# Kernel tuning notes

Hardware: AMD Instinct MI355X
Metric: run time of the kernel (lower is better)

Reference implementation:

```python
import jax, jax.numpy as jnp
import numpy as np

USER_NUM = 100000
ITEM_NUM = 50000
N_NODES = USER_NUM + ITEM_NUM
HIDE_DIM = 64
N_EDGES = 4000000
LAYER_NUM = 3


def setup_inputs() -> dict:
    key = jax.random.key(0)
    k1, k2, k3, k4 = jax.random.split(key, 4)
    # Xavier uniform for embeddings: bound = sqrt(6/(fan_in+fan_out))
    bound_u = float(np.sqrt(6.0 / (USER_NUM + HIDE_DIM)))
    bound_i = float(np.sqrt(6.0 / (ITEM_NUM + HIDE_DIM)))
    user_emb = jax.random.uniform(k1, (USER_NUM, HIDE_DIM), jnp.float32, -bound_u, bound_u)
    item_emb = jax.random.uniform(k2, (ITEM_NUM, HIDE_DIM), jnp.float32, -bound_i, bound_i)
    src = jax.random.randint(k3, (N_EDGES,), 0, N_NODES, dtype=jnp.int32)
    dst = jax.random.randint(k4, (N_EDGES,), 0, N_NODES, dtype=jnp.int32)
    return {"user_emb": user_emb, "item_emb": item_emb, "src": src, "dst": dst}


def _gcn_layer(node_f, src, dst, out_norm, in_norm):
    # node_f: [N, D]; symmetric degree-normalized SpMM (copy_u + sum)
    h = node_f * out_norm  # pre-scale by out_degree^-0.5
    agg = jax.ops.segment_sum(h[src], dst, num_segments=N_NODES)
    return agg * in_norm  # post-scale by in_degree^-0.5


def reference(user_emb, item_emb, src, dst):
    ones = jnp.ones((N_EDGES,), jnp.float32)
    out_deg = jnp.clip(jax.ops.segment_sum(ones, src, num_segments=N_NODES), 1.0)
    in_deg = jnp.clip(jax.ops.segment_sum(ones, dst, num_segments=N_NODES), 1.0)
    out_norm = (out_deg ** -0.5)[:, None]
    in_norm = (in_deg ** -0.5)[:, None]

    res_user = user_emb
    res_item = item_emb
    for i in range(LAYER_NUM):
        if i == 0:
            node_f = jnp.concatenate([res_user, res_item], axis=0)
        else:
            node_f = embeddings
        embeddings = _gcn_layer(node_f, src, dst, out_norm, in_norm)
        scale = 1.0 / (i + 2)
        res_user = res_user + embeddings[:USER_NUM] * scale
        res_item = res_item + embeddings[USER_NUM:] * scale
    return (res_user, res_item)
```

## Files before the change

kernel.cpp:

```cpp
#include <hip/hip_runtime.h>
#include <stdint.h>

#define USER_NUM 100000
#define ITEM_NUM 50000
#define N_NODES  150000
#define HIDE_DIM 64
#define N_EDGES  4000000
#define SLAB     72

#define HRANGES 3
#define RNODES  50000
#define RWORDS  (RNODES / 4)
#define SLICES  128
#define EPS     (N_EDGES / SLICES)

#define BSH     9
#define BNODES  512
#define NBUCK   293
#define SSLICES 640
#define EPSB    (N_EDGES / SSLICES)

__device__ __forceinline__ unsigned short f2bf(float f) {
    union { float f; unsigned int i; } c; c.f = f;
    unsigned int b = c.i;
    return (unsigned short)((b + 0x7FFFu + ((b >> 16) & 1u)) >> 16);
}
__device__ __forceinline__ float lo_bf(uint32_t u) {
    union { uint32_t u; float f; } c; c.u = u << 16; return c.f;
}
__device__ __forceinline__ float hi_bf(uint32_t u) {
    union { uint32_t u; float f; } c; c.u = u & 0xffff0000u; return c.f;
}

__global__ void histfused_kernel(const int* __restrict__ src, const int* __restrict__ dst,
                                 uint32_t* __restrict__ partial, uint32_t* __restrict__ btot) {
    __shared__ uint32_t bins[RWORDS];
    int r  = blockIdx.x / SLICES;
    int sl = blockIdx.x - r * SLICES;
    int e0 = sl * EPS, e1 = e0 + EPS;
    if (r < HRANGES) {
        for (int i = threadIdx.x; i < RWORDS; i += 512) bins[i] = 0;
        __syncthreads();
        int lo = r * RNODES, hi = lo + RNODES;
        for (int e = e0 + threadIdx.x; e < e1; e += 512) {
            int s = src[e];
            if (s >= lo && s < hi) {
                int x = s - lo;
                atomicAdd(&bins[x >> 2], 1u << (8 * (x & 3)));
            }
        }
        __syncthreads();
        uint32_t* out = partial + (size_t)(r * SLICES + sl) * RWORDS;
        for (int i = threadIdx.x; i < RWORDS; i += 512) out[i] = bins[i];
    } else {
        for (int i = threadIdx.x; i < NBUCK; i += 512) bins[i] = 0;
        __syncthreads();
        for (int e = e0 + threadIdx.x; e < e1; e += 512)
            atomicAdd(&bins[((unsigned)dst[e]) >> BSH], 1u);
        __syncthreads();
        for (int i = threadIdx.x; i < NBUCK; i += 512)
            if (bins[i]) atomicAdd(&btot[i], bins[i]);
    }
}

__global__ void rednorm_kernel(const uint32_t* __restrict__ partial, float* __restrict__ out_norm) {
    int g = blockIdx.x * blockDim.x + threadIdx.x;
    if (g >= HRANGES * RWORDS) return;
    int r = g / RWORDS, w = g - r * RWORDS;
    const uint32_t* p = partial + (size_t)r * SLICES * RWORDS + w;
    uint32_t acc = 0;
#pragma unroll 16
    for (int sl = 0; sl < SLICES; ++sl) acc += p[(size_t)sl * RWORDS];
    int oc0 = acc & 255, oc1 = (acc >> 8) & 255, oc2 = (acc >> 16) & 255, oc3 = (acc >> 24);
    float4 o;
    o.x = 1.0f / sqrtf((float)(oc0 < 1 ? 1 : oc0));
    o.y = 1.0f / sqrtf((float)(oc1 < 1 ? 1 : oc1));
    o.z = 1.0f / sqrtf((float)(oc2 < 1 ? 1 : oc2));
    o.w = 1.0f / sqrtf((float)(oc3 < 1 ? 1 : oc3));
    ((float4*)out_norm)[(size_t)r * (RNODES / 4) + w] = o;
}

__global__ void scatter_kernel(const int* __restrict__ src, const int* __restrict__ dst,
                               const uint32_t* __restrict__ btot, uint32_t* __restrict__ gcur,
                               uint32_t* __restrict__ sorted) {
    __shared__ uint32_t cnt[NBUCK];
    __shared__ uint32_t excl[NBUCK];
    __shared__ uint32_t bex[NBUCK];
    __shared__ uint32_t gpos0[NBUCK];
    __shared__ uint32_t sarr[512];
    __shared__ uint32_t sval[EPSB];
    __shared__ uint16_t sbkt[EPSB];

    int s = blockIdx.x;
    int t = threadIdx.x;
    for (int i = t; i < NBUCK; i += 512) cnt[i] = 0;

    uint32_t bv = (t < NBUCK) ? btot[t] : 0;
    sarr[t] = bv;
    __syncthreads();
    for (int off = 1; off < 512; off <<= 1) {
        uint32_t x = (t >= off) ? sarr[t - off] : 0;
        __syncthreads();
        sarr[t] += x;
        __syncthreads();
    }
    if (t < NBUCK) bex[t] = sarr[t] - bv;
    __syncthreads();

    int e0 = s * EPSB;
    for (int e = e0 + t; e < e0 + EPSB; e += 512)
        atomicAdd(&cnt[((unsigned)dst[e]) >> BSH], 1u);
    __syncthreads();

    uint32_t myc = (t < NBUCK) ? cnt[t] : 0;
    sarr[t] = myc;
    __syncthreads();
    for (int off = 1; off < 512; off <<= 1) {
        uint32_t x = (t >= off) ? sarr[t - off] : 0;
        __syncthreads();
        sarr[t] += x;
        __syncthreads();
    }
    if (t < NBUCK) {
        uint32_t ex = sarr[t] - myc;
        excl[t] = ex;
        cnt[t] = ex;
        if (myc) gpos0[t] = bex[t] + atomicAdd(&gcur[t], myc);
    }
    __syncthreads();

    for (int e = e0 + t; e < e0 + EPSB; e += 512) {
        unsigned d = (unsigned)dst[e];
        int sv = src[e];
        unsigned b = d >> BSH;
        unsigned nib = d & (BNODES - 1);
        uint32_t r = atomicAdd(&cnt[b], 1u);
        sval[r] = (uint32_t)sv | (nib << 18);
        sbkt[r] = (uint16_t)b;
    }
    __syncthreads();

    for (int i = t; i < EPSB; i += 512) {
        unsigned b = sbkt[i];
        sorted[gpos0[b] + ((uint32_t)i - excl[b])] = sval[i];
    }
}

__global__ void slab_kernel(const uint32_t* __restrict__ sorted, const uint32_t* __restrict__ btot,
                            int* __restrict__ esrc, int* __restrict__ in_cnt,
                            float* __restrict__ in_norm) {
    __shared__ uint32_t cur[BNODES];
    __shared__ uint32_t sarr[512];
    int b = blockIdx.x;
    int t = threadIdx.x;
    if (t < BNODES) cur[t] = 0;

    uint32_t bv = 0;
    if (t < 512) { bv = (t < NBUCK) ? btot[t] : 0; sarr[t] = bv; }
    __syncthreads();
    for (int off = 1; off < 512; off <<= 1) {
        uint32_t x = 0;
        if (t < 512 && t >= off) x = sarr[t - off];
        __syncthreads();
        if (t < 512) sarr[t] += x;
        __syncthreads();
    }
    uint32_t start = sarr[b] - btot[b];
    uint32_t n = btot[b];

    for (uint32_t i = t; i < n; i += 1024) {
        uint32_t v = sorted[start + i];
        uint32_t nib = v >> 18;
        uint32_t sc = v & 0x3FFFFu;
        uint32_t r = atomicAdd(&cur[nib], 1u);
        if (r < SLAB) esrc[((size_t)(b << BSH) + nib) * SLAB + r] = (int)sc;
    }
    __syncthreads();
    if (t < BNODES) {
        int node = (b << BSH) + t;
        if (node < N_NODES) {
            int ic = (int)cur[t];
            in_cnt[node] = ic;
            if (ic < 1) ic = 1;
            in_norm[node] = 1.0f / sqrtf((float)ic);
        }
    }
}

__global__ void init_kernel(const float2* __restrict__ user2, const float2* __restrict__ item2,
                            const float* __restrict__ out_norm, uint32_t* __restrict__ h0) {
    int gid = blockIdx.x * blockDim.x + threadIdx.x;
    if (gid >= N_NODES * 32) return;
    int node = gid >> 5;
    float2 v = (node < USER_NUM) ? user2[gid] : item2[gid - USER_NUM * 32];
    float on = out_norm[node];
    h0[gid] = (uint32_t)f2bf(v.x * on) | ((uint32_t)f2bf(v.y * on) << 16);
}

__global__ void agg_kernel(const uint32_t* __restrict__ h32, const int* __restrict__ esrc,
                           const int* __restrict__ in_cnt,
                           const float* __restrict__ in_norm, const float* __restrict__ out_norm,
                           const float4* __restrict__ user4, const float4* __restrict__ item4,
                           float4* __restrict__ res4, uint4* __restrict__ hn128,
                           const uint2* __restrict__ h1own,
                           float s1, float s2, float s3, int mode) {
    int wid  = (blockIdx.x * blockDim.x + threadIdx.x) >> 6;
    int lane = threadIdx.x & 63;
    int half = lane >> 5;
    int p    = (lane >> 3) & 3;
    int q    = lane & 7;
    int node = wid * 2 + half;
    if (node >= N_NODES) return;

    int deg = in_cnt[node]; if (deg > SLAB) deg = SLAB;
    int beg = node * SLAB;
    int hb  = half << 5;

    int sl0 = lane & 31;
    int idx0 = (sl0      < deg) ? esrc[beg + sl0]      : 0;
    int idx1 = (sl0 + 32 < deg) ? esrc[beg + sl0 + 32] : 0;

    const uint4* h128 = (const uint4*)h32;

    float a0 = 0.f, a1 = 0.f, a2 = 0.f, a3 = 0.f;
    float a4 = 0.f, a5 = 0.f, a6 = 0.f, a7 = 0.f;

#define ACC8(U) do { \
        a0 += lo_bf((U).x); a1 += hi_bf((U).x); \
        a2 += lo_bf((U).y); a3 += hi_bf((U).y); \
        a4 += lo_bf((U).z); a5 += hi_bf((U).z); \
        a6 += lo_bf((U).w); a7 += hi_bf((U).w); } while (0)

    int d0 = (deg < 32) ? deg : 32;
    {
        int sA0 = __shfl(idx0, hb + p,      64);
        int sA1 = __shfl(idx0, hb + 4 + p,  64);
        int sA2 = __shfl(idx0, hb + 8 + p,  64);
        int sA3 = __shfl(idx0, hb + 12 + p, 64);
        uint4 uA0 = h128[sA0 * 8 + q];
        uint4 uA1 = h128[sA1 * 8 + q];
        uint4 uA2 = h128[sA2 * 8 + q];
        uint4 uA3 = h128[sA3 * 8 + q];
        int sB0 = __shfl(idx0, hb + 16 + p, 64);
        int sB1 = __shfl(idx0, hb + 20 + p, 64);
        int sB2 = __shfl(idx0, hb + 24 + p, 64);
        int sB3 = __shfl(idx0, hb + 28 + p, 64);
        uint4 uB0 = h128[sB0 * 8 + q];
        uint4 uB1 = h128[sB1 * 8 + q];
        uint4 uB2 = h128[sB2 * 8 + q];
        uint4 uB3 = h128[sB3 * 8 + q];
        if (p      < d0) ACC8(uA0);
        if (4 + p  < d0) ACC8(uA1);
        if (8 + p  < d0) ACC8(uA2);
        if (12 + p < d0) ACC8(uA3);
        if (16 + p < d0) ACC8(uB0);
        if (20 + p < d0) ACC8(uB1);
        if (24 + p < d0) ACC8(uB2);
        if (28 + p < d0) ACC8(uB3);
    }

    int m1 = ((deg < 64) ? deg : 64) - 32;
    if (m1 > 0) {
        int nj1 = (m1 + 3) >> 2;
        int j = 0;
        for (; 4 * j + 8 <= m1; j += 2) {
            int e0 = 4 * j + p;
            int s0 = __shfl(idx1, hb + e0,     64);
            int s1g = __shfl(idx1, hb + e0 + 4, 64);
            uint4 u0 = h128[s0 * 8 + q];
            uint4 u1 = h128[s1g * 8 + q];
            ACC8(u0);
            ACC8(u1);
        }
        for (; j < nj1; ++j) {
            int e = 4 * j + p;
            int s = __shfl(idx1, hb + e, 64);
            uint4 u = h128[s * 8 + q];
            if (e < m1) ACC8(u);
        }
    }

    for (int e = 64 + p; e < deg; e += 4) {
        int s = esrc[beg + e];
        uint4 u = h128[s * 8 + q];
        ACC8(u);
    }
#undef ACC8

    a0 += __shfl_xor(a0, 8, 64);  a1 += __shfl_xor(a1, 8, 64);
    a2 += __shfl_xor(a2, 8, 64);  a3 += __shfl_xor(a3, 8, 64);
    a4 += __shfl_xor(a4, 8, 64);  a5 += __shfl_xor(a5, 8, 64);
    a6 += __shfl_xor(a6, 8, 64);  a7 += __shfl_xor(a7, 8, 64);
    a0 += __shfl_xor(a0, 16, 64); a1 += __shfl_xor(a1, 16, 64);
    a2 += __shfl_xor(a2, 16, 64); a3 += __shfl_xor(a3, 16, 64);
    a4 += __shfl_xor(a4, 16, 64); a5 += __shfl_xor(a5, 16, 64);
    a6 += __shfl_xor(a6, 16, 64); a7 += __shfl_xor(a7, 16, 64);

    float innorm = in_norm[node];
    float v0 = a0 * innorm, v1 = a1 * innorm, v2 = a2 * innorm, v3 = a3 * innorm;
    float v4 = a4 * innorm, v5 = a5 * innorm, v6 = a6 * innorm, v7 = a7 * innorm;

    if (mode == 0) {
        if (p == 0) {
            float on = out_norm[node];
            uint4 w;
            w.x = (uint32_t)f2bf(v0 * on) | ((uint32_t)f2bf(v1 * on) << 16);
            w.y = (uint32_t)f2bf(v2 * on) | ((uint32_t)f2bf(v3 * on) << 16);
            w.z = (uint32_t)f2bf(v4 * on) | ((uint32_t)f2bf(v5 * on) << 16);
            w.w = (uint32_t)f2bf(v6 * on) | ((uint32_t)f2bf(v7 * on) << 16);
            hn128[node * 8 + q] = w;
        }
    } else {
        if (p == 1 || p == 2) {
            int of = node * 16 + 2 * q + (p - 1);
            float4 x = (node < USER_NUM) ? user4[of] : item4[of - USER_NUM * 16];
            uint2 h1 = h1own[of];
            uint2 h2 = ((const uint2*)h32)[of];
            float rinv = 1.0f / out_norm[node];
            float b0 = (p == 1) ? v0 : v4;
            float b1 = (p == 1) ? v1 : v5;
            float b2 = (p == 1) ? v2 : v6;
            float b3 = (p == 1) ? v3 : v7;
            float4 rv;
            rv.x = x.x + (lo_bf(h1.x) * s1 + lo_bf(h2.x) * s2) * rinv + b0 * s3;
            rv.y = x.y + (hi_bf(h1.x) * s1 + hi_bf(h2.x) * s2) * rinv + b1 * s3;
            rv.z = x.z + (lo_bf(h1.y) * s1 + lo_bf(h2.y) * s2) * rinv + b2 * s3;
            rv.w = x.w + (hi_bf(h1.y) * s1 + hi_bf(h2.y) * s2) * rinv + b3 * s3;
            res4[of] = rv;
        }
    }
}

static inline uintptr_t align_up(uintptr_t p, uintptr_t a) { return (p + a - 1) & ~(a - 1); }

extern "C" void kernel_launch(void* const* d_in, const int* in_sizes, int n_in,
                              void* d_out, int out_size, void* d_ws, size_t ws_size,
                              hipStream_t stream) {
    const float* user_emb = (const float*)d_in[0];
    const float* item_emb = (const float*)d_in[1];
    const int*   src      = (const int*)d_in[2];
    const int*   dst      = (const int*)d_in[3];
    float*       res      = (float*)d_out;

    uintptr_t p = (uintptr_t)d_ws;
    int* in_cnt = (int*)p;                     p = align_up(p + (size_t)N_NODES * 4, 128);
    float* out_norm = (float*)p;               p = align_up(p + (size_t)N_NODES * 4, 128);
    float* in_norm = (float*)p;                p = align_up(p + (size_t)N_NODES * 4, 128);
    uint32_t* btot = (uint32_t*)p;             p = align_up(p + (size_t)(2 * NBUCK) * 4, 128);
    int* esrc = (int*)p;                       p = align_up(p + (size_t)NBUCK * BNODES * SLAB * 4, 128);
    uint32_t* hA = (uint32_t*)p;               p = align_up(p + (size_t)N_NODES * 32 * 4, 128);
    uint32_t* hB = (uint32_t*)p;
    uint32_t* gcur = btot + NBUCK;
    uint32_t* sorted  = hA;
    uint32_t* partial = hB;

    const int BT = 256;
    int fb = (N_NODES * 32 + BT - 1) / BT;
    int ab = (N_NODES / 2 * 64 + BT - 1) / BT;

    const float2* user2 = (const float2*)user_emb;
    const float2* item2 = (const float2*)item_emb;
    const float4* user4 = (const float4*)user_emb;
    const float4* item4 = (const float4*)item_emb;

    hipMemsetAsync(btot, 0, (size_t)(2 * NBUCK) * 4, stream);
    histfused_kernel<<<(HRANGES + 1) * SLICES, 512, 0, stream>>>(src, dst, partial, btot);
    rednorm_kernel<<<(HRANGES * RWORDS + 255) / 256, 256, 0, stream>>>(partial, out_norm);
    scatter_kernel<<<SSLICES, 512, 0, stream>>>(src, dst, btot, gcur, sorted);
    slab_kernel<<<NBUCK, 1024, 0, stream>>>(sorted, btot, esrc, in_cnt, in_norm);
    init_kernel<<<fb, BT, 0, stream>>>(user2, item2, out_norm, hA);

    agg_kernel<<<ab, BT, 0, stream>>>(hA, esrc, in_cnt, in_norm, out_norm, user4, item4,
                                      (float4*)res, (uint4*)hB, (const uint2*)hB,
                                      0.0f, 0.0f, 0.0f, 0);
    agg_kernel<<<ab, BT, 0, stream>>>(hB, esrc, in_cnt, in_norm, out_norm, user4, item4,
                                      (float4*)res, (uint4*)hA, (const uint2*)hB,
                                      0.0f, 0.0f, 0.0f, 0);
    agg_kernel<<<ab, BT, 0, stream>>>(hA, esrc, in_cnt, in_norm, out_norm, user4, item4,
                                      (float4*)res, (uint4*)hB, (const uint2*)hB,
                                      0.5f, 1.0f / 3.0f, 0.25f, 1);
}
```

Before: 430.9 us.

## Precompute bucket bases once and stage slab writes in LDS for coalesced stores

The prefix scan of bucket totals now runs once, in an extra block of the reduction kernel, instead of being repeated in every scatter and slab block. The slab kernel first counts in-degrees, then builds the padded per-node source lists in shared memory in 128-node chunks and writes them to global memory in contiguous, coalesced stores instead of scattered 4-byte writes. This costs four extra passes over each bucket's sorted edges and a 36KB LDS buffer, which may limit occupancy. It also now writes every slab entry, including the unused padding.

```diff
diff --git a/kernel.cpp b/kernel.cpp
--- a/kernel.cpp
+++ b/kernel.cpp
@@ -13,12 +13,16 @@
 #define RWORDS  (RNODES / 4)
 #define SLICES  128
 #define EPS     (N_EDGES / SLICES)
+#define NRB     ((HRANGES * RWORDS + 511) / 512)
 
 #define BSH     9
 #define BNODES  512
 #define NBUCK   293
 #define SSLICES 640
 #define EPSB    (N_EDGES / SSLICES)
+
+#define CHUNK   128
+#define NCHUNK  (BNODES / CHUNK)
 
 __device__ __forceinline__ unsigned short f2bf(float f) {
     union { float f; unsigned int i; } c; c.f = f;
@@ -63,8 +67,25 @@
     }
 }
 
-__global__ void rednorm_kernel(const uint32_t* __restrict__ partial, float* __restrict__ out_norm) {
-    int g = blockIdx.x * blockDim.x + threadIdx.x;
+__global__ void rednorm_kernel(const uint32_t* __restrict__ partial, float* __restrict__ out_norm,
+                               const uint32_t* __restrict__ btot, uint32_t* __restrict__ bbase) {
+    if (blockIdx.x == NRB) {
+        __shared__ uint32_t tot[512];
+        int t = threadIdx.x;
+        uint32_t v = (t < NBUCK) ? btot[t] : 0;
+        tot[t] = v;
+        __syncthreads();
+        for (int off = 1; off < 512; off <<= 1) {
+            uint32_t x = (t >= off) ? tot[t - off] : 0;
+            __syncthreads();
+            tot[t] += x;
+            __syncthreads();
+        }
+        if (t < NBUCK) bbase[t] = tot[t] - v;
+        if (t == NBUCK - 1) bbase[NBUCK] = tot[t];
+        return;
+    }
+    int g = blockIdx.x * 512 + threadIdx.x;
     if (g >= HRANGES * RWORDS) return;
     int r = g / RWORDS, w = g - r * RWORDS;
     const uint32_t* p = partial + (size_t)r * SLICES * RWORDS + w;
@@ -81,11 +102,10 @@
 }
 
 __global__ void scatter_kernel(const int* __restrict__ src, const int* __restrict__ dst,
-                               const uint32_t* __restrict__ btot, uint32_t* __restrict__ gcur,
+                               const uint32_t* __restrict__ bbase, uint32_t* __restrict__ gcur,
                                uint32_t* __restrict__ sorted) {
     __shared__ uint32_t cnt[NBUCK];
     __shared__ uint32_t excl[NBUCK];
-    __shared__ uint32_t bex[NBUCK];
     __shared__ uint32_t gpos0[NBUCK];
     __shared__ uint32_t sarr[512];
     __shared__ uint32_t sval[EPSB];
@@ -94,17 +114,6 @@
     int s = blockIdx.x;
     int t = threadIdx.x;
     for (int i = t; i < NBUCK; i += 512) cnt[i] = 0;
-
-    uint32_t bv = (t < NBUCK) ? btot[t] : 0;
-    sarr[t] = bv;
-    __syncthreads();
-    for (int off = 1; off < 512; off <<= 1) {
-        uint32_t x = (t >= off) ? sarr[t - off] : 0;
-        __syncthreads();
-        sarr[t] += x;
-        __syncthreads();
-    }
-    if (t < NBUCK) bex[t] = sarr[t] - bv;
     __syncthreads();
 
     int e0 = s * EPSB;
@@ -125,7 +134,7 @@
         uint32_t ex = sarr[t] - myc;
         excl[t] = ex;
         cnt[t] = ex;
-        if (myc) gpos0[t] = bex[t] + atomicAdd(&gcur[t], myc);
+        if (myc) gpos0[t] = bbase[t] + atomicAdd(&gcur[t], myc);
     }
     __syncthreads();
 
@@ -146,44 +155,47 @@
     }
 }
 
-__global__ void slab_kernel(const uint32_t* __restrict__ sorted, const uint32_t* __restrict__ btot,
-                            int* __restrict__ esrc, int* __restrict__ in_cnt,
-                            float* __restrict__ in_norm) {
+__global__ __launch_bounds__(1024) void slab_kernel(
+        const uint32_t* __restrict__ sorted, const uint32_t* __restrict__ btot,
+        const uint32_t* __restrict__ bbase,
+        int* __restrict__ esrc, int* __restrict__ in_cnt, float* __restrict__ in_norm) {
     __shared__ uint32_t cur[BNODES];
-    __shared__ uint32_t sarr[512];
+    __shared__ uint32_t cur2[CHUNK];
+    __shared__ int stage[CHUNK * SLAB];
     int b = blockIdx.x;
     int t = threadIdx.x;
     if (t < BNODES) cur[t] = 0;
-
-    uint32_t bv = 0;
-    if (t < 512) { bv = (t < NBUCK) ? btot[t] : 0; sarr[t] = bv; }
-    __syncthreads();
-    for (int off = 1; off < 512; off <<= 1) {
-        uint32_t x = 0;
-        if (t < 512 && t >= off) x = sarr[t - off];
-        __syncthreads();
-        if (t < 512) sarr[t] += x;
-        __syncthreads();
-    }
-    uint32_t start = sarr[b] - btot[b];
+    __syncthreads();
+    uint32_t start = bbase[b];
     uint32_t n = btot[b];
 
-    for (uint32_t i = t; i < n; i += 1024) {
-        uint32_t v = sorted[start + i];
-        uint32_t nib = v >> 18;
-        uint32_t sc = v & 0x3FFFFu;
-        uint32_t r = atomicAdd(&cur[nib], 1u);
-        if (r < SLAB) esrc[((size_t)(b << BSH) + nib) * SLAB + r] = (int)sc;
-    }
+    for (uint32_t i = t; i < n; i += 1024)
+        atomicAdd(&cur[sorted[start + i] >> 18], 1u);
     __syncthreads();
     if (t < BNODES) {
         int node = (b << BSH) + t;
         if (node < N_NODES) {
             int ic = (int)cur[t];
             in_cnt[node] = ic;
-            if (ic < 1) ic = 1;
-            in_norm[node] = 1.0f / sqrtf((float)ic);
-        }
+            in_norm[node] = 1.0f / sqrtf((float)(ic < 1 ? 1 : ic));
+        }
+    }
+
+    for (int c = 0; c < NCHUNK; ++c) {
+        if (t < CHUNK) cur2[t] = 0;
+        __syncthreads();
+        int lo = c * CHUNK, hi = lo + CHUNK;
+        for (uint32_t i = t; i < n; i += 1024) {
+            uint32_t v = sorted[start + i];
+            int nib = (int)(v >> 18);
+            if (nib >= lo && nib < hi) {
+                uint32_t r = atomicAdd(&cur2[nib - lo], 1u);
+                if (r < SLAB) stage[(nib - lo) * SLAB + r] = (int)(v & 0x3FFFFu);
+            }
+        }
+        __syncthreads();
+        int* dp = esrc + ((size_t)(b << BSH) + lo) * SLAB;
+        for (int i = t; i < CHUNK * SLAB; i += 1024) dp[i] = stage[i];
     }
 }
 
@@ -347,6 +359,7 @@
     float* out_norm = (float*)p;               p = align_up(p + (size_t)N_NODES * 4, 128);
     float* in_norm = (float*)p;                p = align_up(p + (size_t)N_NODES * 4, 128);
     uint32_t* btot = (uint32_t*)p;             p = align_up(p + (size_t)(2 * NBUCK) * 4, 128);
+    uint32_t* bbase = (uint32_t*)p;            p = align_up(p + (size_t)(NBUCK + 1) * 4, 128);
     int* esrc = (int*)p;                       p = align_up(p + (size_t)NBUCK * BNODES * SLAB * 4, 128);
     uint32_t* hA = (uint32_t*)p;               p = align_up(p + (size_t)N_NODES * 32 * 4, 128);
     uint32_t* hB = (uint32_t*)p;
@@ -365,9 +378,9 @@
 
     hipMemsetAsync(btot, 0, (size_t)(2 * NBUCK) * 4, stream);
     histfused_kernel<<<(HRANGES + 1) * SLICES, 512, 0, stream>>>(src, dst, partial, btot);
-    rednorm_kernel<<<(HRANGES * RWORDS + 255) / 256, 256, 0, stream>>>(partial, out_norm);
-    scatter_kernel<<<SSLICES, 512, 0, stream>>>(src, dst, btot, gcur, sorted);
-    slab_kernel<<<NBUCK, 1024, 0, stream>>>(sorted, btot, esrc, in_cnt, in_norm);
+    rednorm_kernel<<<NRB + 1, 512, 0, stream>>>(partial, out_norm, btot, bbase);
+    scatter_kernel<<<SSLICES, 512, 0, stream>>>(src, dst, bbase, gcur, sorted);
+    slab_kernel<<<NBUCK, 1024, 0, stream>>>(sorted, btot, bbase, esrc, in_cnt, in_norm);
     init_kernel<<<fb, BT, 0, stream>>>(user2, item2, out_norm, hA);
 
     agg_kernel<<<ab, BT, 0, stream>>>(hA, esrc, in_cnt, in_norm, out_norm, user4, item4,
```

New measurement: 427.8 us. About the same (-0.7%).
